# Kernel optimization log

Hardware: AMD Instinct MI355X
Metric: run time of the kernel (lower is better)

Reference implementation:

```python
import jax, jax.numpy as jnp
import numpy as np

NUM_HEADS = 8
GROUPS = 32  # min(32, 512 // 4)
EPS = 1e-5


def group_norm(y, gamma, beta):
    B, C, L = y.shape
    yg = y.reshape(B, GROUPS, -1)  # [B, G, (C//G)*L]
    mu = yg.mean(-1, keepdims=True)
    var = yg.var(-1, keepdims=True)
    yn = ((yg - mu) * jax.lax.rsqrt(var + EPS)).reshape(B, C, L)
    return yn * gamma[:, None] + beta[:, None]


def setup_inputs() -> dict:
    key = jax.random.key(0)
    ks = jax.random.split(key, 5)
    B, C, L = 4, 512, 2048
    return {
        "x": jax.random.normal(ks[0], (B, C, L), dtype=jnp.float32),
        "Wqkv": jax.random.normal(ks[1], (3 * C, C), dtype=jnp.float32) * (C ** -0.5),
        "bqkv": jax.random.normal(ks[2], (3 * C,), dtype=jnp.float32) * 0.01,
        "Wproj": jax.random.normal(ks[3], (C, C), dtype=jnp.float32) * (C ** -0.5),
        "bproj": jax.random.normal(ks[4], (C,), dtype=jnp.float32) * 0.01,
        "gamma": jnp.ones((C,), dtype=jnp.float32),
        "beta": jnp.zeros((C,), dtype=jnp.float32),
    }


def reference(x, Wqkv, bqkv, Wproj, bproj, gamma, beta):
    B, C, L = x.shape
    H = NUM_HEADS
    D = C // H
    # 1x1 Conv1d == channel-mixing matmul
    qkv = jnp.einsum('oc,bcl->bol', Wqkv, x) + bqkv[:, None]  # [B, 3C, L]
    qkv = qkv.reshape(B, 3, H, D, L)
    q, k, v = qkv[:, 0], qkv[:, 1], qkv[:, 2]
    q = jnp.clip(q, -10.0, 10.0)
    k = jnp.clip(k, -10.0, 10.0)
    v = jnp.clip(v, -10.0, 10.0)
    scale = D ** -0.5
    attn = jnp.einsum('bhdi,bhdj->bhij', q, k) * scale  # [B, H, L, L]
    attn = jnp.clip(attn, -10.0, 10.0)
    attn = jax.nn.softmax(attn, axis=-1)
    # NaN fallback: replace whole attn with identity if any NaN (matches torch branch)
    has_nan = jnp.isnan(attn).any()
    attn = jnp.where(has_nan, jnp.eye(L, dtype=x.dtype), attn)
    out = jnp.einsum('bhij,bhdj->bhdi', attn, v)  # [B, H, D, L]
    out = out.reshape(B, C, L)
    out = jnp.einsum('oc,bcl->bol', Wproj, out) + bproj[:, None]
    return group_norm(out + x, gamma, beta)
```

## Files before the change

kernel.cpp:

```cpp
#include <hip/hip_runtime.h>
#include <cstddef>

#define B_ 4
#define C_ 512
#define L_ 2048

typedef __attribute__((ext_vector_type(8))) short  short8;
typedef __attribute__((ext_vector_type(4))) float  f32x4;
typedef __attribute__((ext_vector_type(4))) unsigned short us4;

#define AS1 __attribute__((address_space(1)))
#define AS3 __attribute__((address_space(3)))

__device__ __forceinline__ float clip10(float v){ return fminf(fmaxf(v,-10.0f),10.0f); }

__device__ __forceinline__ unsigned short f2bf(float f){
  union { float f; unsigned u; } v; v.f = f;
  unsigned r = v.u + 0x7fffu + ((v.u >> 16) & 1u);
  return (unsigned short)(r >> 16);
}
__device__ __forceinline__ unsigned pk_tr(float lo, float hi){
  return __builtin_amdgcn_perm(__float_as_uint(hi), __float_as_uint(lo), 0x07060302u);
}
__device__ __forceinline__ float bf2f(unsigned short u){
  return __uint_as_float(((unsigned)u)<<16);
}
__device__ __forceinline__ void gl16(const void* g, void* l){
  __builtin_amdgcn_global_load_lds((const AS1 unsigned*)g, (AS3 unsigned*)l, 16, 0, 0);
}
__device__ __forceinline__ void drain_dma(){
  asm volatile("s_waitcnt vmcnt(0)" ::: "memory");
}
__device__ __forceinline__ short8 mk8(unsigned a, unsigned b, unsigned c, unsigned d){
  union { unsigned u[4]; short8 s; } v;
  v.u[0]=a; v.u[1]=b; v.u[2]=c; v.u[3]=d;
  return v.s;
}

__global__ __launch_bounds__(256) void prep_k(
    const float* __restrict__ x, const float* __restrict__ Wq,
    const float* __restrict__ Wp, unsigned short* __restrict__ xT,
    unsigned short* __restrict__ Wqb, unsigned short* __restrict__ Wpb,
    float* __restrict__ part)
{
  const int blk = blockIdx.x;
  const int t = threadIdx.x;
  if (blk < 4096){
    __shared__ float tile[32][33];
    const int b = blk>>10, rem = blk&1023;
    const int c0 = (rem>>6)*32, l0 = (rem&63)*32;
    const int cr = t>>3, lc = (t&7)*4;
    const float4 v = *(const float4*)(x + ((size_t)b*C_ + c0+cr)*L_ + l0 + lc);
    tile[cr][lc]=v.x; tile[cr][lc+1]=v.y; tile[cr][lc+2]=v.z; tile[cr][lc+3]=v.w;
    __syncthreads();
    const int lr = t>>3, cc = (t&7)*4;
    const us4 o = { f2bf(tile[cc][lr]), f2bf(tile[cc+1][lr]),
                    f2bf(tile[cc+2][lr]), f2bf(tile[cc+3][lr]) };
    *(us4*)(xT + ((size_t)b*L_ + l0+lr)*C_ + c0 + cc) = o;
  } else if (blk < 5120){
    const int i = (blk-4096)*256 + t;
    const int NQ = 1536*512/4;
    const float* src; unsigned short* dst; int j;
    if (i < NQ){ src = Wq; dst = Wqb; j = i; }
    else       { src = Wp; dst = Wpb; j = i - NQ; }
    const float4 v = *(const float4*)(src + (size_t)j*4);
    const us4 o = { f2bf(v.x), f2bf(v.y), f2bf(v.z), f2bf(v.w) };
    *(us4*)(dst + (size_t)j*4) = o;
  } else {
    part[t] = 0.f;
  }
}

template<int MODE>
__global__ __launch_bounds__(256) void mfma_gemm(
    const unsigned short* __restrict__ Wb, const unsigned short* __restrict__ Bin,
    const float* __restrict__ bias, const float* __restrict__ xres,
    unsigned short* __restrict__ qT, unsigned short* __restrict__ kT,
    unsigned short* __restrict__ vN,
    float* __restrict__ part)
{
  __shared__ unsigned short SA[128*64];
  __shared__ unsigned short SB[128*64];
  const int t = threadIdx.x;
  const int b = blockIdx.z;
  const int mb = blockIdx.y, n0 = blockIdx.x*128, m0 = mb*128;
  const int lane = t&63, w = t>>6, wm = w>>1, wn = w&1;
  const int n = lane&15, q4 = lane>>4;
  const bool SWAP = (MODE==1) || (MODE==0 && mb>=8);

  f32x4 acc[4][4];
#pragma unroll
  for (int i=0;i<4;i++)
#pragma unroll
    for (int j=0;j<4;j++) acc[i][j] = (f32x4){0.f,0.f,0.f,0.f};

  const unsigned short* Arow = Wb + (size_t)m0*512;
  const unsigned short* Brow = Bin + ((size_t)b*L_ + n0)*512;

  for (int kt=0; kt<8; kt++){
    const int k0 = kt*64;
    __syncthreads();
#pragma unroll
    for (int i=0;i<4;i++){
      const int ch = t + 256*i;
      const int row = ch>>3, lc = (ch&7) ^ (row&7);
      gl16(Arow + (size_t)row*512 + k0 + lc*8, &SA[ch*8]);
      gl16(Brow + (size_t)row*512 + k0 + lc*8, &SB[ch*8]);
    }
    drain_dma();
    __syncthreads();
#pragma unroll
    for (int kk=0;kk<2;kk++){
      short8 aF[4], bF[4];
      const int pc = ((kk*4+q4) ^ (n&7))*8;
#pragma unroll
      for (int mt=0;mt<4;mt++) aF[mt] = *(const short8*)&SA[(wm*64+mt*16+n)*64 + pc];
#pragma unroll
      for (int nt=0;nt<4;nt++) bF[nt] = *(const short8*)&SB[(wn*64+nt*16+n)*64 + pc];
      if (SWAP){
#pragma unroll
        for (int mt=0;mt<4;mt++)
#pragma unroll
          for (int nt=0;nt<4;nt++)
            acc[mt][nt] = __builtin_amdgcn_mfma_f32_16x16x32_bf16(bF[nt], aF[mt], acc[mt][nt], 0,0,0);
      } else {
#pragma unroll
        for (int mt=0;mt<4;mt++)
#pragma unroll
          for (int nt=0;nt<4;nt++)
            acc[mt][nt] = __builtin_amdgcn_mfma_f32_16x16x32_bf16(aF[mt], bF[nt], acc[mt][nt], 0,0,0);
      }
    }
  }

  const float QS = 0.180336880f;
  if (MODE==0 && SWAP){
#pragma unroll
    for (int mt=0;mt<4;mt++){
      const int o = m0 + wm*64 + mt*16 + n;
      const float bv = bias[o];
#pragma unroll
      for (int nt=0;nt<4;nt++){
        const int p = ((nt>>1)<<2) | ((q4&1)<<3) | ((q4>>1)<<4) | ((nt&1)<<5);
        const int l = n0 + wn*64 + p;
        const float r0=clip10(acc[mt][nt][0]+bv), r1=clip10(acc[mt][nt][1]+bv),
                    r2=clip10(acc[mt][nt][2]+bv), r3=clip10(acc[mt][nt][3]+bv);
        const us4 ov = { f2bf(r0), f2bf(r1), f2bf(r2), f2bf(r3) };
        *(us4*)&vN[((size_t)b*512 + (o-1024))*L_ + l] = ov;
      }
    }
    return;
  }
  if (MODE==1){
#pragma unroll
    for (int mt=0;mt<4;mt++){
      const int o = m0 + wm*64 + mt*16 + n;
      const float bv = bias[o];
      float gs=0.f, gq=0.f;
#pragma unroll
      for (int nt=0;nt<4;nt++){
        const int l = n0 + wn*64 + nt*16 + q4*4;
        const float4 xv = *(const float4*)(xres + ((size_t)b*512 + o)*L_ + l);
        const float y0=acc[mt][nt][0]+bv+xv.x, y1=acc[mt][nt][1]+bv+xv.y,
                    y2=acc[mt][nt][2]+bv+xv.z, y3=acc[mt][nt][3]+bv+xv.w;
        gs += (y0+y1)+(y2+y3);
        gq += (y0*y0+y1*y1)+(y2*y2+y3*y3);
        const us4 ov = { f2bf(y0), f2bf(y1), f2bf(y2), f2bf(y3) };
        *(us4*)&vN[((size_t)b*512 + o)*L_ + l] = ov;
      }
#pragma unroll
      for (int off=1; off<64; off<<=1){
        gs += __shfl_xor(gs, off);
        gq += __shfl_xor(gq, off);
      }
      if (lane==0){
        const int g = mb*8 + wm*4 + mt;
        atomicAdd(&part[(b*32+g)*2+0], gs);
        atomicAdd(&part[(b*32+g)*2+1], gq);
      }
    }
    return;
  }
#pragma unroll
  for (int mt=0;mt<4;mt++){
    const int obase = m0 + wm*64 + mt*16 + q4*4;
    const float b0=bias[obase], b1=bias[obase+1], b2=bias[obase+2], b3=bias[obase+3];
#pragma unroll
    for (int nt=0;nt<4;nt++){
      const int l = n0 + wn*64 + nt*16 + n;
      float r0=clip10(acc[mt][nt][0]+b0), r1=clip10(acc[mt][nt][1]+b1),
            r2=clip10(acc[mt][nt][2]+b2), r3=clip10(acc[mt][nt][3]+b3);
      const int typ = mb>>2;
      const int oin = obase - typ*512;
      if (typ==0){ r0*=QS; r1*=QS; r2*=QS; r3*=QS; }
      unsigned short* dst = (typ==0) ? qT : kT;
      const us4 o = { f2bf(r0), f2bf(r1), f2bf(r2), f2bf(r3) };
      *(us4*)&dst[((size_t)b*L_ + l)*512 + oin] = o;
    }
  }
}

#define OPX 68
#define PPITCH 21

__global__ __launch_bounds__(1024,8) void attn_v17(
    const unsigned short* __restrict__ qT, const unsigned short* __restrict__ kT,
    const unsigned short* __restrict__ vN,
    unsigned short* __restrict__ attnT)
{
  __shared__ unsigned short smem[32768];
  const int t  = threadIdx.x;
  const int id  = blockIdx.x;
  const int xcd = id & 7, s = id >> 3;
  const int pr  = xcd*4 + (s & 3);
  const int i0  = (s >> 2) * 128;
  const int h   = pr & 7, b = pr >> 3;
  const int lane = t&63, w = t>>6, n = lane&15, q4 = lane>>4;
  const int iw = w & 7;
  const int jg = w >> 3;
  const int jbase = jg*1024;

  const unsigned short* kb0 = kT + (size_t)b*L_*512 + h*64;
  const unsigned short* vb  = vN + ((size_t)b*512 + h*64)*L_;

  short8 qf[2];
#pragma unroll
  for (int kk=0; kk<2; kk++)
    qf[kk] = *(const short8*)(qT + ((size_t)b*L_ + i0 + iw*16 + n)*512
                                 + h*64 + kk*32 + q4*8);

  short8 ones;
#pragma unroll
  for (int i=0;i<8;i++) ones[i] = (short)0x3F80;

  const f32x4 ZC = (f32x4){0.f,0.f,0.f,0.f};

  f32x4 oacc[4];
  f32x4 oden = (f32x4){0.f,0.f,0.f,0.f};
#pragma unroll
  for (int dt=0;dt<4;dt++) oacc[dt]=(f32x4){0.f,0.f,0.f,0.f};

  const float LIM = 14.4269504089f;

  const int pcA = (q4 ^ (n&7))*8;
  const int pcB = ((4+q4) ^ (n&7))*8;

  const int tg = t & 511;
  const int srow = tg>>3, slc = (tg&7)^(srow&7);
  unsigned short* gbase = &smem[jg*16384];
  const unsigned short* kp = kb0 + (size_t)(jbase+srow)*512 + slc*8;
  const unsigned short* vp = vb + (size_t)srow*L_ + jbase + slc*8;

  gl16(kp, &gbase[tg*8]);
  gl16(vp, &gbase[4096 + tg*8]);
  kp += 64*512; vp += 64;
  drain_dma();
  __syncthreads();

  for (int jt=0; jt<16; jt++){
    const int cur = jt&1;
    const unsigned short* sk = &gbase[cur*8192];
    const unsigned short* sv = &gbase[cur*8192 + 4096];

    if (jt < 15){
      unsigned short* nb = &gbase[(cur^1)*8192];
      gl16(kp, &nb[tg*8]);
      gl16(vp, &nb[4096 + tg*8]);
      kp += 64*512; vp += 64;
    }

    f32x4 sacc[4];
    {
      short8 aK[4];
#pragma unroll
      for (int j4=0;j4<4;j4++) aK[j4] = *(const short8*)&sk[(j4*16+n)*64 + pcA];
#pragma unroll
      for (int j4=0;j4<4;j4++)
        sacc[j4] = __builtin_amdgcn_mfma_f32_16x16x32_bf16(aK[j4], qf[0], ZC, 0,0,0);
#pragma unroll
      for (int j4=0;j4<4;j4++) aK[j4] = *(const short8*)&sk[(j4*16+n)*64 + pcB];
#pragma unroll
      for (int j4=0;j4<4;j4++)
        sacc[j4] = __builtin_amdgcn_mfma_f32_16x16x32_bf16(aK[j4], qf[1], sacc[j4], 0,0,0);
    }

    unsigned pw[4][2];
#pragma unroll
    for (int j4=0;j4<4;j4++){
      const float e0 = __builtin_amdgcn_exp2f(__builtin_amdgcn_fmed3f(sacc[j4][0],-LIM,LIM));
      const float e1 = __builtin_amdgcn_exp2f(__builtin_amdgcn_fmed3f(sacc[j4][1],-LIM,LIM));
      const float e2 = __builtin_amdgcn_exp2f(__builtin_amdgcn_fmed3f(sacc[j4][2],-LIM,LIM));
      const float e3 = __builtin_amdgcn_exp2f(__builtin_amdgcn_fmed3f(sacc[j4][3],-LIM,LIM));
      pw[j4][0] = pk_tr(e0,e1);
      pw[j4][1] = pk_tr(e2,e3);
    }

#pragma unroll
    for (int kk=0;kk<2;kk++){
      const int pcv = kk ? pcB : pcA;
      short8 bV[4];
#pragma unroll
      for (int dt=0;dt<4;dt++) bV[dt] = *(const short8*)&sv[(dt*16+n)*64 + pcv];
      const short8 pA = mk8(pw[kk][0], pw[kk][1], pw[kk+2][0], pw[kk+2][1]);
#pragma unroll
      for (int dt=0;dt<4;dt++)
        oacc[dt] = __builtin_amdgcn_mfma_f32_16x16x32_bf16(pA, bV[dt], oacc[dt], 0,0,0);
      oden = __builtin_amdgcn_mfma_f32_16x16x32_bf16(pA, ones, oden, 0,0,0);
    }
    drain_dma();
    __syncthreads();
  }

  float* pbuf = (float*)smem;
  if (jg == 1){
    const int slot = (iw*64 + lane)*PPITCH;
#pragma unroll
    for (int dt=0;dt<4;dt++)
#pragma unroll
      for (int r=0;r<4;r++) pbuf[slot + dt*4 + r] = oacc[dt][r];
#pragma unroll
    for (int r=0;r<4;r++) pbuf[slot + 16 + r] = oden[r];
  }
  __syncthreads();
  if (jg == 1) return;

  {
    const int slot = (iw*64 + lane)*PPITCH;
#pragma unroll
    for (int dt=0;dt<4;dt++)
#pragma unroll
      for (int r=0;r<4;r++) oacc[dt][r] += pbuf[slot + dt*4 + r];
#pragma unroll
    for (int r=0;r<4;r++) oden[r] += pbuf[slot + 16 + r];
  }

  float inv[4];
#pragma unroll
  for (int r=0;r<4;r++) inv[r] = 1.0f/oden[r];

  unsigned short* sb = &smem[21504];
#pragma unroll
  for (int dt=0;dt<4;dt++)
#pragma unroll
    for (int r=0;r<4;r++)
      sb[(iw*16 + q4*4 + r)*OPX + dt*16 + n] = f2bf(oacc[dt][r]*inv[r]);
#pragma unroll
  for (int it=0; it<4; it++){
    const int chunk = it*64 + lane;
    const int row = chunk>>4, c4 = (chunk&15)*4;
    const us4 ov = *(const us4*)&sb[(iw*16 + row)*OPX + c4];
    *(us4*)&attnT[((size_t)b*L_ + i0 + iw*16 + row)*512 + h*64 + c4] = ov;
  }
}

__global__ __launch_bounds__(256) void gn_apply(
    const unsigned short* __restrict__ yb, const float* __restrict__ part,
    const float* __restrict__ gamma, const float* __restrict__ beta,
    float* __restrict__ out)
{
  const int blk = blockIdx.x;
  const int b = blk>>7, g = (blk>>2)&31, s = blk&3;
  const float sum = part[(b*32+g)*2+0];
  const float sq  = part[(b*32+g)*2+1];
  const float mu = sum*(1.0f/32768.0f);
  const float rs = rsqrtf(sq*(1.0f/32768.0f) - mu*mu + 1e-5f);
  const size_t base = ((size_t)b*C_ + g*16)*L_ + s*512;
  const int t = threadIdx.x;
#pragma unroll
  for (int i=0;i<4;i++){
    const int chunk = i*256 + t;
    const int row = chunk>>6;
    const int lc  = (chunk&63)*8;
    const int c = g*16 + row;
    const float ga = gamma[c]*rs, be = beta[c] - mu*ga;
    const size_t off = base + (size_t)row*L_ + lc;
    const short8 v = *(const short8*)(yb + off);
    float4 r1, r2;
    r1.x = bf2f((unsigned short)v[0])*ga + be;
    r1.y = bf2f((unsigned short)v[1])*ga + be;
    r1.z = bf2f((unsigned short)v[2])*ga + be;
    r1.w = bf2f((unsigned short)v[3])*ga + be;
    r2.x = bf2f((unsigned short)v[4])*ga + be;
    r2.y = bf2f((unsigned short)v[5])*ga + be;
    r2.z = bf2f((unsigned short)v[6])*ga + be;
    r2.w = bf2f((unsigned short)v[7])*ga + be;
    *(float4*)(out+off)   = r1;
    *(float4*)(out+off+4) = r2;
  }
}

extern "C" void kernel_launch(void* const* d_in, const int* in_sizes, int n_in,
                              void* d_out, int out_size, void* d_ws, size_t ws_size,
                              hipStream_t stream)
{
  (void)in_sizes; (void)n_in; (void)out_size; (void)ws_size;
  const float* x     = (const float*)d_in[0];
  const float* Wqkv  = (const float*)d_in[1];
  const float* bqkv  = (const float*)d_in[2];
  const float* Wproj = (const float*)d_in[3];
  const float* bproj = (const float*)d_in[4];
  const float* gamma = (const float*)d_in[5];
  const float* beta  = (const float*)d_in[6];
  float* out = (float*)d_out;
  char* ws = (char*)d_ws;

  const size_t MB = 1024*1024;
  unsigned short* qT    = (unsigned short*)(ws);
  unsigned short* kT    = (unsigned short*)(ws +  8*MB);
  unsigned short* vN    = (unsigned short*)(ws + 16*MB);
  unsigned short* attnT = (unsigned short*)(ws + 24*MB);
  unsigned short* xT    = (unsigned short*)(ws + 32*MB);
  unsigned short* Wqb   = (unsigned short*)(ws + 42*MB);
  unsigned short* Wpb   = (unsigned short*)(ws + 44*MB);
  unsigned short* yb    = (unsigned short*)(ws + 45*MB);
  float*          part  = (float*)        (ws + 61*MB);

  prep_k      <<<dim3(5121),   256,0,stream>>>(x, Wqkv, Wproj, xT, Wqb, Wpb, part);
  mfma_gemm<0><<<dim3(16,12,4),256,0,stream>>>(Wqb, xT,    bqkv , nullptr, qT,kT,vN, nullptr);
  attn_v17    <<<dim3(512),   1024,0,stream>>>(qT, kT, vN, attnT);
  mfma_gemm<1><<<dim3(16, 4,4),256,0,stream>>>(Wpb, attnT, bproj, x, nullptr,nullptr, yb, part);
  gn_apply    <<<dim3(512),    256,0,stream>>>(yb, part, gamma, beta, out);
}
```

Measured before the change: 176.4 us.

## Double query rows per attention block to reuse K/V tiles across two M-tiles

Each wave of the attention kernel now handles 32 query rows (two 16-row M-tiles) instead of 16, so each block covers 256 queries and the grid shrinks from 512 to 256 blocks. Every K and V fragment loaded from LDS is reused for twice as many MFMAs, halving K/V global and LDS traffic per query. The cost is more accumulator registers (launch bounds relaxed from 8 to 4 waves per SIMD) and fewer blocks on the GPU, which may reduce occupancy and load balance. The cross-group partial-sum reduction is also split into two passes with extra barriers.

After: 178.9 us. No clear change (+1.4%).

```diff
diff --git a/kernel.cpp b/kernel.cpp
--- a/kernel.cpp
+++ b/kernel.cpp
@@ -203,7 +203,7 @@
 #define OPX 68
 #define PPITCH 21
 
-__global__ __launch_bounds__(1024,8) void attn_v17(
+__global__ __launch_bounds__(1024,4) void attn_v18(
     const unsigned short* __restrict__ qT, const unsigned short* __restrict__ kT,
     const unsigned short* __restrict__ vN,
     unsigned short* __restrict__ attnT)
@@ -213,7 +213,7 @@
   const int id  = blockIdx.x;
   const int xcd = id & 7, s = id >> 3;
   const int pr  = xcd*4 + (s & 3);
-  const int i0  = (s >> 2) * 128;
+  const int i0  = (s >> 2) * 256;
   const int h   = pr & 7, b = pr >> 3;
   const int lane = t&63, w = t>>6, n = lane&15, q4 = lane>>4;
   const int iw = w & 7;
@@ -223,22 +223,24 @@
   const unsigned short* kb0 = kT + (size_t)b*L_*512 + h*64;
   const unsigned short* vb  = vN + ((size_t)b*512 + h*64)*L_;
 
-  short8 qf[2];
-#pragma unroll
-  for (int kk=0; kk<2; kk++)
-    qf[kk] = *(const short8*)(qT + ((size_t)b*L_ + i0 + iw*16 + n)*512
-                                 + h*64 + kk*32 + q4*8);
+  short8 qf[2][2];
+#pragma unroll
+  for (int mt=0; mt<2; mt++)
+#pragma unroll
+    for (int kk=0; kk<2; kk++)
+      qf[mt][kk] = *(const short8*)(qT + ((size_t)b*L_ + i0 + iw*32 + mt*16 + n)*512
+                                       + h*64 + kk*32 + q4*8);
 
   short8 ones;
 #pragma unroll
   for (int i=0;i<8;i++) ones[i] = (short)0x3F80;
 
-  const f32x4 ZC = (f32x4){0.f,0.f,0.f,0.f};
-
-  f32x4 oacc[4];
-  f32x4 oden = (f32x4){0.f,0.f,0.f,0.f};
-#pragma unroll
-  for (int dt=0;dt<4;dt++) oacc[dt]=(f32x4){0.f,0.f,0.f,0.f};
+  f32x4 oacc[2][4];
+  f32x4 oden[2];
+#pragma unroll
+  for (int mt=0;mt<2;mt++){ oden[mt]=(f32x4){0.f,0.f,0.f,0.f};
+#pragma unroll
+    for (int dt=0;dt<4;dt++) oacc[mt][dt]=(f32x4){0.f,0.f,0.f,0.f}; }
 
   const float LIM = 14.4269504089f;
 
@@ -269,31 +271,39 @@
       kp += 64*512; vp += 64;
     }
 
-    f32x4 sacc[4];
+    f32x4 sacc[2][4];
     {
       short8 aK[4];
 #pragma unroll
       for (int j4=0;j4<4;j4++) aK[j4] = *(const short8*)&sk[(j4*16+n)*64 + pcA];
 #pragma unroll
-      for (int j4=0;j4<4;j4++)
-        sacc[j4] = __builtin_amdgcn_mfma_f32_16x16x32_bf16(aK[j4], qf[0], ZC, 0,0,0);
+      for (int mt=0;mt<2;mt++)
+#pragma unroll
+        for (int j4=0;j4<4;j4++)
+          sacc[mt][j4] = __builtin_amdgcn_mfma_f32_16x16x32_bf16(
+              aK[j4], qf[mt][0], (f32x4){0.f,0.f,0.f,0.f}, 0,0,0);
 #pragma unroll
       for (int j4=0;j4<4;j4++) aK[j4] = *(const short8*)&sk[(j4*16+n)*64 + pcB];
 #pragma unroll
-      for (int j4=0;j4<4;j4++)
-        sacc[j4] = __builtin_amdgcn_mfma_f32_16x16x32_bf16(aK[j4], qf[1], sacc[j4], 0,0,0);
-    }
-
-    unsigned pw[4][2];
-#pragma unroll
-    for (int j4=0;j4<4;j4++){
-      const float e0 = __builtin_amdgcn_exp2f(__builtin_amdgcn_fmed3f(sacc[j4][0],-LIM,LIM));
-      const float e1 = __builtin_amdgcn_exp2f(__builtin_amdgcn_fmed3f(sacc[j4][1],-LIM,LIM));
-      const float e2 = __builtin_amdgcn_exp2f(__builtin_amdgcn_fmed3f(sacc[j4][2],-LIM,LIM));
-      const float e3 = __builtin_amdgcn_exp2f(__builtin_amdgcn_fmed3f(sacc[j4][3],-LIM,LIM));
-      pw[j4][0] = pk_tr(e0,e1);
-      pw[j4][1] = pk_tr(e2,e3);
-    }
+      for (int mt=0;mt<2;mt++)
+#pragma unroll
+        for (int j4=0;j4<4;j4++)
+          sacc[mt][j4] = __builtin_amdgcn_mfma_f32_16x16x32_bf16(
+              aK[j4], qf[mt][1], sacc[mt][j4], 0,0,0);
+    }
+
+    unsigned pw[2][4][2];
+#pragma unroll
+    for (int mt=0;mt<2;mt++)
+#pragma unroll
+      for (int j4=0;j4<4;j4++){
+        const float e0 = __builtin_amdgcn_exp2f(__builtin_amdgcn_fmed3f(sacc[mt][j4][0],-LIM,LIM));
+        const float e1 = __builtin_amdgcn_exp2f(__builtin_amdgcn_fmed3f(sacc[mt][j4][1],-LIM,LIM));
+        const float e2 = __builtin_amdgcn_exp2f(__builtin_amdgcn_fmed3f(sacc[mt][j4][2],-LIM,LIM));
+        const float e3 = __builtin_amdgcn_exp2f(__builtin_amdgcn_fmed3f(sacc[mt][j4][3],-LIM,LIM));
+        pw[mt][j4][0] = pk_tr(e0,e1);
+        pw[mt][j4][1] = pk_tr(e2,e3);
+      }
 
 #pragma unroll
     for (int kk=0;kk<2;kk++){
@@ -301,55 +311,66 @@
       short8 bV[4];
 #pragma unroll
       for (int dt=0;dt<4;dt++) bV[dt] = *(const short8*)&sv[(dt*16+n)*64 + pcv];
-      const short8 pA = mk8(pw[kk][0], pw[kk][1], pw[kk+2][0], pw[kk+2][1]);
+#pragma unroll
+      for (int mt=0;mt<2;mt++){
+        const short8 pA = mk8(pw[mt][kk][0], pw[mt][kk][1],
+                              pw[mt][kk+2][0], pw[mt][kk+2][1]);
+#pragma unroll
+        for (int dt=0;dt<4;dt++)
+          oacc[mt][dt] = __builtin_amdgcn_mfma_f32_16x16x32_bf16(pA, bV[dt], oacc[mt][dt], 0,0,0);
+        oden[mt] = __builtin_amdgcn_mfma_f32_16x16x32_bf16(pA, ones, oden[mt], 0,0,0);
+      }
+    }
+    drain_dma();
+    __syncthreads();
+  }
+
+  float* pbuf = (float*)smem;
+#pragma unroll
+  for (int mt=0;mt<2;mt++){
+    if (jg == 1){
+      const int slot = (iw*64 + lane)*PPITCH;
 #pragma unroll
       for (int dt=0;dt<4;dt++)
-        oacc[dt] = __builtin_amdgcn_mfma_f32_16x16x32_bf16(pA, bV[dt], oacc[dt], 0,0,0);
-      oden = __builtin_amdgcn_mfma_f32_16x16x32_bf16(pA, ones, oden, 0,0,0);
-    }
-    drain_dma();
-    __syncthreads();
-  }
-
-  float* pbuf = (float*)smem;
-  if (jg == 1){
-    const int slot = (iw*64 + lane)*PPITCH;
+#pragma unroll
+        for (int r=0;r<4;r++) pbuf[slot + dt*4 + r] = oacc[mt][dt][r];
+#pragma unroll
+      for (int r=0;r<4;r++) pbuf[slot + 16 + r] = oden[mt][r];
+    }
+    __syncthreads();
+    if (jg == 0){
+      const int slot = (iw*64 + lane)*PPITCH;
+#pragma unroll
+      for (int dt=0;dt<4;dt++)
+#pragma unroll
+        for (int r=0;r<4;r++) oacc[mt][dt][r] += pbuf[slot + dt*4 + r];
+#pragma unroll
+      for (int r=0;r<4;r++) oden[mt][r] += pbuf[slot + 16 + r];
+    }
+    __syncthreads();
+  }
+  if (jg == 1) return;
+
+  float inv[2][4];
+#pragma unroll
+  for (int mt=0;mt<2;mt++)
+#pragma unroll
+    for (int r=0;r<4;r++) inv[mt][r] = 1.0f/oden[mt][r];
+
+  unsigned short* sb = smem;
+#pragma unroll
+  for (int mt=0;mt<2;mt++)
 #pragma unroll
     for (int dt=0;dt<4;dt++)
 #pragma unroll
-      for (int r=0;r<4;r++) pbuf[slot + dt*4 + r] = oacc[dt][r];
-#pragma unroll
-    for (int r=0;r<4;r++) pbuf[slot + 16 + r] = oden[r];
-  }
-  __syncthreads();
-  if (jg == 1) return;
-
-  {
-    const int slot = (iw*64 + lane)*PPITCH;
-#pragma unroll
-    for (int dt=0;dt<4;dt++)
-#pragma unroll
-      for (int r=0;r<4;r++) oacc[dt][r] += pbuf[slot + dt*4 + r];
-#pragma unroll
-    for (int r=0;r<4;r++) oden[r] += pbuf[slot + 16 + r];
-  }
-
-  float inv[4];
-#pragma unroll
-  for (int r=0;r<4;r++) inv[r] = 1.0f/oden[r];
-
-  unsigned short* sb = &smem[21504];
-#pragma unroll
-  for (int dt=0;dt<4;dt++)
-#pragma unroll
-    for (int r=0;r<4;r++)
-      sb[(iw*16 + q4*4 + r)*OPX + dt*16 + n] = f2bf(oacc[dt][r]*inv[r]);
-#pragma unroll
-  for (int it=0; it<4; it++){
+      for (int r=0;r<4;r++)
+        sb[(iw*32 + mt*16 + q4*4 + r)*OPX + dt*16 + n] = f2bf(oacc[mt][dt][r]*inv[mt][r]);
+#pragma unroll
+  for (int it=0; it<8; it++){
     const int chunk = it*64 + lane;
     const int row = chunk>>4, c4 = (chunk&15)*4;
-    const us4 ov = *(const us4*)&sb[(iw*16 + row)*OPX + c4];
-    *(us4*)&attnT[((size_t)b*L_ + i0 + iw*16 + row)*512 + h*64 + c4] = ov;
+    const us4 ov = *(const us4*)&sb[(iw*32 + row)*OPX + c4];
+    *(us4*)&attnT[((size_t)b*L_ + i0 + iw*32 + row)*512 + h*64 + c4] = ov;
   }
 }
 
@@ -417,7 +438,7 @@
 
   prep_k      <<<dim3(5121),   256,0,stream>>>(x, Wqkv, Wproj, xT, Wqb, Wpb, part);
   mfma_gemm<0><<<dim3(16,12,4),256,0,stream>>>(Wqb, xT,    bqkv , nullptr, qT,kT,vN, nullptr);
-  attn_v17    <<<dim3(512),   1024,0,stream>>>(qT, kT, vN, attnT);
+  attn_v18    <<<dim3(256),   1024,0,stream>>>(qT, kT, vN, attnT);
   mfma_gemm<1><<<dim3(16, 4,4),256,0,stream>>>(Wpb, attnT, bproj, x, nullptr,nullptr, yb, part);
   gn_apply    <<<dim3(512),    256,0,stream>>>(yb, part, gamma, beta, out);
 }
```
